# Kernel optimization log

Measured on AMD Instinct MI355X. Metric: run time of the kernel, lower is better.

The kernel has to match this reference:

```python
import jax, jax.numpy as jnp
import numpy as np

N_QUBITS = 16
N_LAYERS = 4
N_ACTIONS = 6
BATCH = 512


def _apply_1q(state, U, wire):
    """Apply a single-qubit gate U to `wire` of batched state [B,2,...,2].
    U is [2,2] (shared) or [B,2,2] (per-sample)."""
    s = jnp.moveaxis(state, wire + 1, -1)
    if U.ndim == 2:
        s = jnp.einsum('ij,b...j->b...i', U, s)
    else:
        s = jnp.einsum('bij,b...j->b...i', U, s)
    return jnp.moveaxis(s, -1, wire + 1)


def _ry(theta):
    # RY(theta); theta scalar or [B]
    c = jnp.cos(theta / 2).astype(jnp.complex64)
    s = jnp.sin(theta / 2).astype(jnp.complex64)
    return jnp.stack([jnp.stack([c, -s], -1), jnp.stack([s, c], -1)], -2)


def _rot(phi, theta, omega):
    # PennyLane Rot = RZ(omega) RY(theta) RZ(phi)
    c = jnp.cos(theta / 2)
    s = jnp.sin(theta / 2)
    ep = jnp.exp(-0.5j * (phi + omega).astype(jnp.complex64))
    em = jnp.exp(-0.5j * (phi - omega).astype(jnp.complex64))
    m00 = ep * c
    m01 = -jnp.conj(em) * s
    m10 = em * s
    m11 = jnp.conj(ep) * c
    return jnp.stack([jnp.stack([m00, m01], -1), jnp.stack([m10, m11], -1)], -2)


def _cz_factor(wire):
    # diagonal CZ phase on wires (wire, wire+1): diag(1,1,1,-1)
    f = jnp.array([1, 1, 1, -1], dtype=jnp.complex64).reshape(2, 2)
    shape = (1,) + (1,) * wire + (2, 2) + (1,) * (N_QUBITS - wire - 2)
    return f.reshape(shape)


def _circuit(x, weights):
    # x: [B, n_qubits] angles; weights: [L, n_qubits, 3]
    B = x.shape[0]
    state = jnp.zeros((B,) + (2,) * N_QUBITS, dtype=jnp.complex64)
    state = state.at[(slice(None),) + (0,) * N_QUBITS].set(1.0)
    # AngleEmbedding: RY(x_i) on wire i (per-sample angles)
    for i in range(N_QUBITS):
        state = _apply_1q(state, _ry(x[:, i]), i)
    for l in range(N_LAYERS):
        for i in range(N_QUBITS):
            state = _apply_1q(state, _rot(weights[l, i, 0], weights[l, i, 1], weights[l, i, 2]), i)
        for i in range(N_QUBITS - 1):
            state = state * _cz_factor(i)
    probs = state.real ** 2 + state.imag ** 2  # [B,2,...,2]
    zs = []
    all_axes = tuple(range(1, N_QUBITS + 1))
    for i in range(N_QUBITS):
        pi = jnp.sum(probs, axis=tuple(a for a in all_axes if a != i + 1))  # [B,2]
        zs.append(pi[:, 0] - pi[:, 1])
    return jnp.stack(zs, axis=-1)  # [B, n_qubits] expval <Z_i>


def setup_inputs() -> dict:
    key = jax.random.key(0)
    k1, k2, k3, k4 = jax.random.split(key, 4)
    x = jax.random.uniform(k1, (BATCH, N_QUBITS), dtype=jnp.float32) * np.float32(np.pi)
    weights = jax.random.normal(k2, (N_LAYERS, N_QUBITS, 3), dtype=jnp.float32)
    fc_w = jax.random.normal(k3, (N_ACTIONS, N_QUBITS), dtype=jnp.float32) / np.float32(np.sqrt(N_QUBITS))
    fc_b = jax.random.normal(k4, (N_ACTIONS,), dtype=jnp.float32) * 0.01
    return {"x": x, "weights": weights, "fc_w": fc_w, "fc_b": fc_b}


def reference(x, weights, fc_w, fc_b):
    z = _circuit(x, weights).astype(jnp.float32)  # [B, n_qubits]
    return z @ fc_w.T + fc_b  # [B, n_actions]
```

## Files before the change

kernel.cpp:

```cpp
#include <hip/hip_runtime.h>

#define NQ 16
#define NL 4
#define NA 6
#define BATCH 512


__global__ __launch_bounds__(1024, 8)
void qdqn_one_kernel(const float* __restrict__ x,
                     const float* __restrict__ wt,
                     const float* __restrict__ fw,
                     const float* __restrict__ fb,
                     float* __restrict__ out)
{
    __shared__ float4 lm[4][NQ][2];
    __shared__ float zsh[NQ];

    const int tid = threadIdx.x;
    const int b   = blockIdx.x;

    if (tid < 64) {
        const int w = tid & 15;
        const int g = tid >> 4;
        float4 R0, R1;
        if (g == 0) {
            const float phi = wt[w * 3 + 0], th = wt[w * 3 + 1];
            float sp, cp, st, ct, sx, cx;
            sincosf(0.5f * phi, &sp, &cp);
            sincosf(0.5f * th,  &st, &ct);
            sincosf(0.5f * x[b * NQ + w], &sx, &cx);
            const float w00r =  ct * cp, w00i = -ct * sp;
            const float w01r = -st * cp, w01i = -st * sp;
            const float w10r =  st * cp, w10i = -st * sp;
            const float w11r =  ct * cp, w11i =  ct * sp;
            R0 = make_float4( w00r*cx + w01r*sx,  w00i*cx + w01i*sx,
                             -w00r*sx + w01r*cx, -w00i*sx + w01i*cx);
            R1 = make_float4(-w10r*sx + w11r*cx, -w10i*sx + w11i*cx,
                              w10r*cx + w11r*sx,  w10i*cx + w11i*sx);
        } else {
            const float al = wt[((g - 1) * NQ + w) * 3 + 2] + wt[(g * NQ + w) * 3 + 0];
            const float th = wt[(g * NQ + w) * 3 + 1];
            float sa, ca, st, ct;
            sincosf(0.5f * al, &sa, &ca);
            sincosf(0.5f * th, &st, &ct);
            R0 = make_float4(ct * ca, -ct * sa, -st * ca, -st * sa);
            R1 = make_float4(ct * ca,  ct * sa,  st * ca, -st * sa);
        }
        lm[g][w][0] = R0;
        lm[g][w][1] = R1;
    }
    __syncthreads();

    const int lane = tid & 63;
    const int qi   = tid >> 6;

    float ar0 = (lane == 0) ? 1.0f : 0.0f, ai0 = 0.0f;
    float ar1 = 0.0f, ai1 = 0.0f;

    const int n0 = lane << 1, n1 = n0 | 1;
    const float czs0 = (__popc((n0 & (n0 >> 1)) & 0x3F) & 1) ? -1.0f : 1.0f;
    const float czs1 = (__popc((n1 & (n1 >> 1)) & 0x3F) & 1) ? -1.0f : 1.0f;

#define GATE(J, G) do {                                                        \
    const int w_ = qi + (J) - 3;                                               \
    if (0 <= w_ && w_ < NQ) {                                \
        if ((J) == 0) {                                                        \
            const float4 r0 = lm[G][w_][0], r1 = lm[G][w_][1];                 \
            const float nr0 = r0.x*ar0 - r0.y*ai0 + r0.z*ar1 - r0.w*ai1;       \
            const float ni0 = r0.x*ai0 + r0.y*ar0 + r0.z*ai1 + r0.w*ar1;       \
            const float nr1 = r1.z*ar0 - r1.w*ai0 + r1.x*ar1 - r1.y*ai1;       \
            const float ni1 = r1.z*ai0 + r1.w*ar0 + r1.x*ai1 + r1.y*ar1;       \
            ar0 = nr0; ai0 = ni0; ar1 = nr1; ai1 = ni1;                        \
        } else {                                                               \
            const int m_   = 1 << ((J) - 1);                                   \
            const int row_ = (lane >> ((J) - 1)) & 1;                          \
            const float4 c = lm[G][w_][row_];                                  \
            const float pr0 = __shfl_xor(ar0, m_, 64);                         \
            const float pi0 = __shfl_xor(ai0, m_, 64);                         \
            const float pr1 = __shfl_xor(ar1, m_, 64);                         \
            const float pi1 = __shfl_xor(ai1, m_, 64);                         \
            const float t0r = c.x*ar0 - c.y*ai0 + c.z*pr0 - c.w*pi0;           \
            const float t0i = c.x*ai0 + c.y*ar0 + c.z*pi0 + c.w*pr0;           \
            const float t1r = c.x*ar1 - c.y*ai1 + c.z*pr1 - c.w*pi1;           \
            const float t1i = c.x*ai1 + c.y*ar1 + c.z*pi1 + c.w*pr1;           \
            ar0 = t0r; ai0 = t0i; ar1 = t1r; ai1 = t1i;                        \
        }                                                                      \
    }                                                                          \
} while (0)

#define CZ() do { ar0 *= czs0; ai0 *= czs0; ar1 *= czs1; ai1 *= czs1; } while (0)

    GATE(0,0); GATE(1,0); GATE(2,0); GATE(3,0); GATE(4,0); GATE(5,0); GATE(6,0);
    CZ();
    GATE(1,1); GATE(2,1); GATE(3,1); GATE(4,1); GATE(5,1);
    CZ();
    GATE(2,2); GATE(3,2); GATE(4,2);
    CZ();
    GATE(3,3);

#undef GATE
#undef CZ

    const float sm = ((lane >> 2) & 1) ? -1.0f : 1.0f;
    float p = sm * (ar0*ar0 + ai0*ai0 + ar1*ar1 + ai1*ai1);
#pragma unroll
    for (int off = 32; off > 0; off >>= 1)
        p += __shfl_xor(p, off, 64);
    if (lane == 0) zsh[qi] = p;
    __syncthreads();

    if (tid < NA) {
        float acc = fb[tid];
#pragma unroll
        for (int i = 0; i < NQ; ++i)
            acc += zsh[i] * fw[tid * NQ + i];
        out[b * NA + tid] = acc;
    }
}

extern "C" void kernel_launch(void* const* d_in, const int* in_sizes, int n_in,
                              void* d_out, int out_size, void* d_ws, size_t ws_size,
                              hipStream_t stream) {
    const float* x    = (const float*)d_in[0];
    const float* wts  = (const float*)d_in[1];
    const float* fc_w = (const float*)d_in[2];
    const float* fc_b = (const float*)d_in[3];
    float* out = (float*)d_out;

    qdqn_one_kernel<<<BATCH, 1024, 0, stream>>>(x, wts, fc_w, fc_b, out);
}
```

Baseline: 66.50 us.

## Initialize light-cone state as product state and fold final Rot into Z measurement

Builds the first-layer state directly as a tensor product of per-qubit single-qubit vectors, so the 7 gate applications with shuffles are replaced by a few complex multiplies. The last layer's rotation is folded into a rotated Z observable, computed with one shuffle and a bilinear form instead of a gate application. Boundary wires get padded identity entries, which removes the per-gate bounds branches. It also switches to fast __sincosf intrinsics and spreads the setup across four wavefronts, trading some precision in the angles for cheaper math.

```diff
diff --git a/kernel.cpp b/kernel.cpp
--- a/kernel.cpp
+++ b/kernel.cpp
@@ -1,108 +1,146 @@
 #include <hip/hip_runtime.h>
 
 #define NQ 16
-#define NL 4
 #define NA 6
 #define BATCH 512
 
 
 __global__ __launch_bounds__(1024, 8)
-void qdqn_one_kernel(const float* __restrict__ x,
-                     const float* __restrict__ wt,
-                     const float* __restrict__ fw,
-                     const float* __restrict__ fb,
-                     float* __restrict__ out)
+void qdqn_kernel(const float* __restrict__ x,
+                 const float* __restrict__ wt,
+                 const float* __restrict__ fw,
+                 const float* __restrict__ fb,
+                 float* __restrict__ out)
 {
-    __shared__ float4 lm[4][NQ][2];
-    __shared__ float zsh[NQ];
+    __shared__ float4 vec[22];
+    __shared__ float4 g2[22][2];
+    __shared__ float4 g3[22][2];
+    __shared__ float4 meas[16];
+    __shared__ float  zsh[NQ];
 
-    const int tid = threadIdx.x;
-    const int b   = blockIdx.x;
+    const int tid  = threadIdx.x;
+    const int b    = blockIdx.x;
+    const int lane = tid & 63;
+    const int wv   = tid >> 6;
 
-    if (tid < 64) {
-        const int w = tid & 15;
-        const int g = tid >> 4;
-        float4 R0, R1;
-        if (g == 0) {
-            const float phi = wt[w * 3 + 0], th = wt[w * 3 + 1];
-            float sp, cp, st, ct, sx, cx;
-            sincosf(0.5f * phi, &sp, &cp);
-            sincosf(0.5f * th,  &st, &ct);
-            sincosf(0.5f * x[b * NQ + w], &sx, &cx);
-            const float w00r =  ct * cp, w00i = -ct * sp;
-            const float w01r = -st * cp, w01i = -st * sp;
-            const float w10r =  st * cp, w10i = -st * sp;
-            const float w11r =  ct * cp, w11i =  ct * sp;
-            R0 = make_float4( w00r*cx + w01r*sx,  w00i*cx + w01i*sx,
-                             -w00r*sx + w01r*cx, -w00i*sx + w01i*cx);
-            R1 = make_float4(-w10r*sx + w11r*cx, -w10i*sx + w11i*cx,
-                              w10r*cx + w11r*sx,  w10i*cx + w11i*sx);
-        } else {
-            const float al = wt[((g - 1) * NQ + w) * 3 + 2] + wt[(g * NQ + w) * 3 + 0];
-            const float th = wt[(g * NQ + w) * 3 + 1];
-            float sa, ca, st, ct;
-            sincosf(0.5f * al, &sa, &ca);
-            sincosf(0.5f * th, &st, &ct);
-            R0 = make_float4(ct * ca, -ct * sa, -st * ca, -st * sa);
-            R1 = make_float4(ct * ca,  ct * sa,  st * ca, -st * sa);
+    if (wv == 0) {
+        if (lane < 22) {
+            const int w = lane - 3;
+            float4 r = make_float4(1.0f, 0.0f, 0.0f, 0.0f);
+            if (0 <= w && w < NQ) {
+                float sp, cp, st, ct, sx, cx;
+                __sincosf(0.5f * wt[w * 3 + 0], &sp, &cp);
+                __sincosf(0.5f * wt[w * 3 + 1], &st, &ct);
+                __sincosf(0.5f * x[b * NQ + w], &sx, &cx);
+                r = make_float4(cp * (ct * cx - st * sx), -sp * (ct * cx + st * sx),
+                                cp * (st * cx + ct * sx),  sp * (ct * sx - st * cx));
+            }
+            vec[lane] = r;
         }
-        lm[g][w][0] = R0;
-        lm[g][w][1] = R1;
+    } else if (wv == 1) {
+        if (lane < 22) {
+            const int w = lane - 3;
+            float4 R0 = make_float4(1.0f, 0.0f, 0.0f, 0.0f);
+            float4 R1 = make_float4(1.0f, 0.0f, 0.0f, 0.0f);
+            if (0 <= w && w < NQ) {
+                const float al = wt[(0 * NQ + w) * 3 + 2] + wt[(1 * NQ + w) * 3 + 0];
+                const float th = wt[(1 * NQ + w) * 3 + 1];
+                float sa, ca, st, ct;
+                __sincosf(0.5f * al, &sa, &ca);
+                __sincosf(0.5f * th, &st, &ct);
+                R0 = make_float4(ct * ca, -ct * sa, -st * ca, -st * sa);
+                R1 = make_float4(ct * ca,  ct * sa,  st * ca, -st * sa);
+            }
+            g2[lane][0] = R0; g2[lane][1] = R1;
+        }
+    } else if (wv == 2) {
+        if (lane < 22) {
+            const int w = lane - 3;
+            float4 R0 = make_float4(1.0f, 0.0f, 0.0f, 0.0f);
+            float4 R1 = make_float4(1.0f, 0.0f, 0.0f, 0.0f);
+            if (0 <= w && w < NQ) {
+                const float al = wt[(1 * NQ + w) * 3 + 2] + wt[(2 * NQ + w) * 3 + 0];
+                const float th = wt[(2 * NQ + w) * 3 + 1];
+                float sa, ca, st, ct;
+                __sincosf(0.5f * al, &sa, &ca);
+                __sincosf(0.5f * th, &st, &ct);
+                R0 = make_float4(ct * ca, -ct * sa, -st * ca, -st * sa);
+                R1 = make_float4(ct * ca,  ct * sa,  st * ca, -st * sa);
+            }
+            g3[lane][0] = R0; g3[lane][1] = R1;
+        }
+    } else if (wv == 3) {
+        if (lane < NQ) {
+            const int w = lane;
+            const float th = wt[(3 * NQ + w) * 3 + 1];
+            const float al = wt[(2 * NQ + w) * 3 + 2] + wt[(3 * NQ + w) * 3 + 0];
+            float s4, c4, sa, ca;
+            __sincosf(th, &s4, &c4);
+            __sincosf(al, &sa, &ca);
+            meas[w] = make_float4(c4, -s4 * ca, -s4 * sa, 0.0f);
+        }
     }
     __syncthreads();
 
-    const int lane = tid & 63;
-    const int qi   = tid >> 6;
+    const int qi = wv;
 
-    float ar0 = (lane == 0) ? 1.0f : 0.0f, ai0 = 0.0f;
-    float ar1 = 0.0f, ai1 = 0.0f;
+    float Pr, Pi;
+    {
+        const float2* vp = reinterpret_cast<const float2*>(vec);
+        float2 f = vp[((qi + 1) << 1) + (lane & 1)];
+        Pr = f.x; Pi = f.y;
+#pragma unroll
+        for (int j = 2; j <= 6; ++j) {
+            const float2 g = vp[((qi + j) << 1) + ((lane >> (j - 1)) & 1)];
+            const float nr = Pr * g.x - Pi * g.y;
+            const float ni = Pr * g.y + Pi * g.x;
+            Pr = nr; Pi = ni;
+        }
+    }
+    const float4 v0 = vec[qi];
+    float ar0 = Pr * v0.x - Pi * v0.y, ai0 = Pr * v0.y + Pi * v0.x;
+    float ar1 = Pr * v0.z - Pi * v0.w, ai1 = Pr * v0.w + Pi * v0.z;
 
     const int n0 = lane << 1, n1 = n0 | 1;
     const float czs0 = (__popc((n0 & (n0 >> 1)) & 0x3F) & 1) ? -1.0f : 1.0f;
     const float czs1 = (__popc((n1 & (n1 >> 1)) & 0x3F) & 1) ? -1.0f : 1.0f;
 
-#define GATE(J, G) do {                                                        \
-    const int w_ = qi + (J) - 3;                                               \
-    if (0 <= w_ && w_ < NQ) {                                \
-        if ((J) == 0) {                                                        \
-            const float4 r0 = lm[G][w_][0], r1 = lm[G][w_][1];                 \
-            const float nr0 = r0.x*ar0 - r0.y*ai0 + r0.z*ar1 - r0.w*ai1;       \
-            const float ni0 = r0.x*ai0 + r0.y*ar0 + r0.z*ai1 + r0.w*ar1;       \
-            const float nr1 = r1.z*ar0 - r1.w*ai0 + r1.x*ar1 - r1.y*ai1;       \
-            const float ni1 = r1.z*ai0 + r1.w*ar0 + r1.x*ai1 + r1.y*ar1;       \
-            ar0 = nr0; ai0 = ni0; ar1 = nr1; ai1 = ni1;                        \
-        } else {                                                               \
-            const int m_   = 1 << ((J) - 1);                                   \
-            const int row_ = (lane >> ((J) - 1)) & 1;                          \
-            const float4 c = lm[G][w_][row_];                                  \
-            const float pr0 = __shfl_xor(ar0, m_, 64);                         \
-            const float pi0 = __shfl_xor(ai0, m_, 64);                         \
-            const float pr1 = __shfl_xor(ar1, m_, 64);                         \
-            const float pi1 = __shfl_xor(ai1, m_, 64);                         \
-            const float t0r = c.x*ar0 - c.y*ai0 + c.z*pr0 - c.w*pi0;           \
-            const float t0i = c.x*ai0 + c.y*ar0 + c.z*pi0 + c.w*pr0;           \
-            const float t1r = c.x*ar1 - c.y*ai1 + c.z*pr1 - c.w*pi1;           \
-            const float t1i = c.x*ai1 + c.y*ar1 + c.z*pi1 + c.w*pr1;           \
-            ar0 = t0r; ai0 = t0i; ar1 = t1r; ai1 = t1i;                        \
-        }                                                                      \
-    }                                                                          \
+#define CZ() do { ar0 *= czs0; ai0 *= czs0; ar1 *= czs1; ai1 *= czs1; } while (0)
+#define GATE(J, ARR) do {                                                      \
+    const int  m_   = 1 << ((J) - 1);                                          \
+    const int  row_ = (lane >> ((J) - 1)) & 1;                                 \
+    const float4 c  = ARR[qi + (J)][row_];                                     \
+    const float pr0 = __shfl_xor(ar0, m_, 64);                                 \
+    const float pi0 = __shfl_xor(ai0, m_, 64);                                 \
+    const float pr1 = __shfl_xor(ar1, m_, 64);                                 \
+    const float pi1 = __shfl_xor(ai1, m_, 64);                                 \
+    const float t0r = c.x*ar0 - c.y*ai0 + c.z*pr0 - c.w*pi0;                   \
+    const float t0i = c.x*ai0 + c.y*ar0 + c.z*pi0 + c.w*pr0;                   \
+    const float t1r = c.x*ar1 - c.y*ai1 + c.z*pr1 - c.w*pi1;                   \
+    const float t1i = c.x*ai1 + c.y*ar1 + c.z*pi1 + c.w*pr1;                   \
+    ar0 = t0r; ai0 = t0i; ar1 = t1r; ai1 = t1i;                                \
 } while (0)
 
-#define CZ() do { ar0 *= czs0; ai0 *= czs0; ar1 *= czs1; ai1 *= czs1; } while (0)
-
-    GATE(0,0); GATE(1,0); GATE(2,0); GATE(3,0); GATE(4,0); GATE(5,0); GATE(6,0);
     CZ();
-    GATE(1,1); GATE(2,1); GATE(3,1); GATE(4,1); GATE(5,1);
+    GATE(1, g2); GATE(2, g2); GATE(3, g2); GATE(4, g2); GATE(5, g2);
     CZ();
-    GATE(2,2); GATE(3,2); GATE(4,2);
+    GATE(2, g3); GATE(3, g3); GATE(4, g3);
     CZ();
-    GATE(3,3);
 
 #undef GATE
 #undef CZ
 
-    const float sm = ((lane >> 2) & 1) ? -1.0f : 1.0f;
-    float p = sm * (ar0*ar0 + ai0*ai0 + ar1*ar1 + ai1*ai1);
+    const float4 m  = meas[qi];
+    const float sgn3 = ((lane >> 2) & 1) ? -1.0f : 1.0f;
+    const float pr0 = __shfl_xor(ar0, 4, 64);
+    const float pi0 = __shfl_xor(ai0, 4, 64);
+    const float pr1 = __shfl_xor(ar1, 4, 64);
+    const float pi1 = __shfl_xor(ai1, 4, 64);
+    const float u  = ar0 * pr0 + ai0 * pi0 + ar1 * pr1 + ai1 * pi1;
+    const float v  = ar0 * pi0 - ai0 * pr0 + ar1 * pi1 - ai1 * pr1;
+    float p = sgn3 * (m.x * (ar0*ar0 + ai0*ai0 + ar1*ar1 + ai1*ai1) - m.z * v)
+            + m.y * u;
+
 #pragma unroll
     for (int off = 32; off > 0; off >>= 1)
         p += __shfl_xor(p, off, 64);
@@ -127,5 +165,5 @@
     const float* fc_b = (const float*)d_in[3];
     float* out = (float*)d_out;
 
-    qdqn_one_kernel<<<BATCH, 1024, 0, stream>>>(x, wts, fc_w, fc_b, out);
+    qdqn_kernel<<<BATCH, 1024, 0, stream>>>(x, wts, fc_w, fc_b, out);
 }
```

Measured after the change: 63.90 us. 3.9% less time.
